# Optimization experiments

Measured on AMD Instinct MI355X. Metric: run time of the kernel, lower is better.

The kernel has to match this reference:

```python
import jax, jax.numpy as jnp
import numpy as np

B, D, H, W = 32, 64, 32, 32   # batch, laten_dim, latent spatial dims
K = 2048                      # codebook_size


def setup_inputs() -> dict:
    key = jax.random.key(0)
    k1, k2 = jax.random.split(key)
    laten = jax.random.normal(k1, (B, D, H, W), dtype=jnp.float32)
    codebook = jax.random.normal(k2, (K, D), dtype=jnp.float32)
    return {"laten": laten, "codebook": codebook}


def reference(laten, codebook):
    # Faithful jax translation of VQVAE.quant_laten.
    b, c, h, w = laten.shape
    # (b, c, h, w) -> (b*h*w, c)
    x = jnp.transpose(laten, (0, 2, 3, 1)).reshape(-1, c)  # (N, D)
    # avoids materializing the (N, K, D) broadcast intermediate.
    x_sq = jnp.sum(x * x, axis=-1, keepdims=True)          # (N, 1)
    e_sq = jnp.sum(codebook * codebook, axis=-1)           # (K,)
    l2_distance = (x_sq - 2.0 * (x @ codebook.T) + e_sq) / c  # (N, K)
    closest_idx_2d = jnp.argmin(l2_distance, axis=-1).reshape(b, h, w)
    # gather + permute(0, 3, 1, 2)
    quant_laten = jnp.transpose(codebook[closest_idx_2d], (0, 3, 1, 2))
    return closest_idx_2d, quant_laten
```

## Files before the change

kernel.cpp:

```cpp
#include <hip/hip_runtime.h>

#define N_PIX 32768
#define DIM   64
#define KCODE 2048

typedef __attribute__((ext_vector_type(8))) short bf16x8;
typedef __attribute__((ext_vector_type(4))) float f32x4;

__device__ inline unsigned short f2bf(float v) {
    unsigned int u = __float_as_uint(v);
    return (unsigned short)((u + 0x7FFFu + ((u >> 16) & 1u)) >> 16);
}
__device__ inline float bf2f(unsigned short b) {
    return __uint_as_float(((unsigned int)b) << 16);
}

__global__ __launch_bounds__(256)
void convert_b_kernel(const float* __restrict__ cb, unsigned short* __restrict__ Bg,
                      float* __restrict__ esq) {
    const int t   = blockIdx.x * 256 + threadIdx.x;
    const int n   = t >> 4;
    const int sub = t & 15;
    const int ntile = n >> 4, ni = n & 15;

    const float4 v = *(const float4*)(cb + (size_t)n * DIM + sub * 4);

    unsigned int h01, h23, m01, m23, l01, l23;
    {
        unsigned short h, m, l;
        float r1;
        h = f2bf(v.x); r1 = v.x - bf2f(h); m = f2bf(r1); l = f2bf(r1 - bf2f(m));
        h01 = h;       m01 = m;       l01 = l;
        h = f2bf(v.y); r1 = v.y - bf2f(h); m = f2bf(r1); l = f2bf(r1 - bf2f(m));
        h01 |= (unsigned int)h << 16; m01 |= (unsigned int)m << 16; l01 |= (unsigned int)l << 16;
        h = f2bf(v.z); r1 = v.z - bf2f(h); m = f2bf(r1); l = f2bf(r1 - bf2f(m));
        h23 = h;       m23 = m;       l23 = l;
        h = f2bf(v.w); r1 = v.w - bf2f(h); m = f2bf(r1); l = f2bf(r1 - bf2f(m));
        h23 |= (unsigned int)h << 16; m23 |= (unsigned int)m << 16; l23 |= (unsigned int)l << 16;
    }

    float s = (v.x * v.x + v.y * v.y) + (v.z * v.z + v.w * v.w);
#pragma unroll
    for (int mk = 1; mk < 16; mk <<= 1) s += __shfl_xor(s, mk, 16);
    if (sub == 0) esq[n] = s;

    char* outb = (char*)Bg;
    const size_t u = ((((size_t)ntile) * 8 + (sub >> 1)) << 8) + ni * 16 + (sub & 1) * 8;
    uint2 hw2 = {h01, h23}, mw2 = {m01, m23}, lw2 = {l01, l23};
    *(uint2*)(outb + u)          = hw2;
    *(uint2*)(outb + 262144 + u) = mw2;
    *(uint2*)(outb + 524288 + u) = lw2;
}

#define DO_PASS(APL, BPL)                                                    \
    _Pragma("unroll") for (int ks = 0; ks < 2; ++ks)                         \
    _Pragma("unroll") for (int mt = 0; mt < 4; ++mt)                         \
        acc[mt] = __builtin_amdgcn_mfma_f32_16x16x32_bf16(                   \
            af[APL][mt][ks], bfr[BPL][ks], acc[mt], 0, 0, 0);

#define RELOAD(PL, JN)                                                       \
    if ((JN) < 32) {                                                         \
      const char* gb = bp0 + (size_t)(JN) * 2048 + (size_t)(PL) * 262144;    \
      bfr[PL][0] = *(const bf16x8*)(gb);                                     \
      bfr[PL][1] = *(const bf16x8*)(gb + 1024);                              \
    }

#define ITER(J)                                                              \
  {                                                                          \
    f32x4 acc[4];                                                            \
    acc[0] = f32x4{0.f, 0.f, 0.f, 0.f};                                      \
    acc[1] = f32x4{0.f, 0.f, 0.f, 0.f};                                      \
    acc[2] = f32x4{0.f, 0.f, 0.f, 0.f};                                      \
    acc[3] = f32x4{0.f, 0.f, 0.f, 0.f};                                      \
    __builtin_amdgcn_s_setprio(1);                                           \
    DO_PASS(0, 2)                                                            \
    RELOAD(2, (J) + 1)                                                       \
    DO_PASS(2, 0)                                                            \
    DO_PASS(1, 1)                                                            \
    DO_PASS(0, 1)                                                            \
    RELOAD(1, (J) + 1)                                                       \
    DO_PASS(1, 0)                                                            \
    DO_PASS(0, 0)                                                            \
    RELOAD(0, (J) + 1)                                                       \
    __builtin_amdgcn_s_setprio(0);                                           \
    const int n = wn * 512 + (J) * 16 + col;                                 \
    const float e = esqS[n];                                                 \
    _Pragma("unroll") for (int mt = 0; mt < 4; ++mt)                         \
    _Pragma("unroll") for (int r = 0; r < 4; ++r) {                          \
      float d = fmaf(-2.f, acc[mt][r], e);                                   \
      if (d < best[mt][r]) { best[mt][r] = d; bidx[mt][r] = n; }             \
    }                                                                        \
  }

__global__ __launch_bounds__(256, 2)
void dist_fused_kernel(const float* __restrict__ laten,
                       const unsigned short* __restrict__ Bg,
                       const float* __restrict__ esq,
                       const float* __restrict__ cb,
                       float* __restrict__ out0, float* __restrict__ out1) {
    __shared__ __align__(16) char ring[24576];
    __shared__ float esqS[2048];

    const int tid  = threadIdx.x;
    const int lane = tid & 63;
    const int wn   = tid >> 6;
    const int quad = lane >> 4, col = lane & 15;
    const int bx = blockIdx.x;
    const int bb = bx >> 4, hw0 = (bx & 15) * 64;

    const char* BgB = (const char*)Bg;
    const char* bp0 = BgB + (size_t)(wn * 32) * 2048 + lane * 16;

    {
        const int p = tid & 63, dgp = tid >> 6;
        const int mt = p >> 4, mi = p & 15;
#pragma unroll
        for (int dd = 0; dd < 2; ++dd) {
            const int dg = dgp * 2 + dd;
            const float* srcA = laten + (size_t)bb * 65536 + (size_t)dg * 8192 + hw0 + p;
            alignas(16) unsigned short hv[8], mv[8], lv[8];
#pragma unroll
            for (int j = 0; j < 8; ++j) {
                float v = srcA[(size_t)j << 10];
                unsigned short h = f2bf(v);
                float r1 = v - bf2f(h);
                unsigned short m = f2bf(r1);
                unsigned short l = f2bf(r1 - bf2f(m));
                hv[j] = h; mv[j] = m; lv[j] = l;
            }
            int u = ((mt * 8 + dg) << 8) + mi * 16;
            *(uint4*)(ring + u)         = *(uint4*)hv;
            *(uint4*)(ring + 8192 + u)  = *(uint4*)mv;
            *(uint4*)(ring + 16384 + u) = *(uint4*)lv;
        }
    }
    *(float4*)(esqS + tid * 8)     = *(const float4*)(esq + tid * 8);
    *(float4*)(esqS + tid * 8 + 4) = *(const float4*)(esq + tid * 8 + 4);
    __syncthreads();

    bf16x8 af[3][4][2];
#pragma unroll
    for (int pl = 0; pl < 3; ++pl)
#pragma unroll
        for (int mt = 0; mt < 4; ++mt)
#pragma unroll
            for (int ks = 0; ks < 2; ++ks)
                af[pl][mt][ks] = *(const bf16x8*)(ring + pl * 8192
                    + ((mt * 8 + ks * 4 + quad) << 8) + col * 16);
    __syncthreads();

    bf16x8 bfr[3][2];
    RELOAD(2, 0)
    RELOAD(0, 0)
    RELOAD(1, 0)

    float best[4][4];
    int   bidx[4][4];
#pragma unroll
    for (int mt = 0; mt < 4; ++mt)
#pragma unroll
        for (int r = 0; r < 4; ++r) { best[mt][r] = 3.4e38f; bidx[mt][r] = 0; }

    for (int j = 0; j < 32; ++j) ITER(j)

    float* redD = (float*)ring;
    int*   redI = (int*)(ring + 1024);
    int*   idxF = (int*)(ring + 2048);
#pragma unroll
    for (int mt = 0; mt < 4; ++mt)
#pragma unroll
        for (int r = 0; r < 4; ++r) {
            float d = best[mt][r];
            int   i = bidx[mt][r];
#pragma unroll
            for (int m = 1; m < 16; m <<= 1) {
                float od = __shfl_xor(d, m, 16);
                int   oi = __shfl_xor(i, m, 16);
                if (od < d || (od == d && oi < i)) { d = od; i = oi; }
            }
            if (col == 0) {
                int row = mt * 16 + quad * 4 + r;
                redD[row * 4 + wn] = d;
                redI[row * 4 + wn] = i;
            }
        }
    __syncthreads();

    if (tid < 64) {
        float bd = redD[tid * 4]; int bi = redI[tid * 4];
#pragma unroll
        for (int w = 1; w < 4; ++w) {
            float d = redD[tid * 4 + w]; int i = redI[tid * 4 + w];
            if (d < bd || (d == bd && i < bi)) { bd = d; bi = i; }
        }
        out0[bx * 64 + tid] = (float)bi;
        idxF[tid] = bi;
    }
    __syncthreads();

    const int p = tid & 63, dgp = tid >> 6;
    const int idx = idxF[p];
    const float4* srcr = (const float4*)(cb + ((size_t)idx << 6) + dgp * 16);
    float* o = out1 + (size_t)bb * 65536 + (size_t)dgp * 16384 + hw0 + p;
    float4 v0 = srcr[0], v1 = srcr[1], v2 = srcr[2], v3 = srcr[3];
    o[(size_t)0  << 10] = v0.x; o[(size_t)1  << 10] = v0.y;
    o[(size_t)2  << 10] = v0.z; o[(size_t)3  << 10] = v0.w;
    o[(size_t)4  << 10] = v1.x; o[(size_t)5  << 10] = v1.y;
    o[(size_t)6  << 10] = v1.z; o[(size_t)7  << 10] = v1.w;
    o[(size_t)8  << 10] = v2.x; o[(size_t)9  << 10] = v2.y;
    o[(size_t)10 << 10] = v2.z; o[(size_t)11 << 10] = v2.w;
    o[(size_t)12 << 10] = v3.x; o[(size_t)13 << 10] = v3.y;
    o[(size_t)14 << 10] = v3.z; o[(size_t)15 << 10] = v3.w;
}

extern "C" void kernel_launch(void* const* d_in, const int* in_sizes, int n_in,
                              void* d_out, int out_size, void* d_ws, size_t ws_size,
                              hipStream_t stream) {
    const float* laten = (const float*)d_in[0];
    const float* cb    = (const float*)d_in[1];

    float* out0 = (float*)d_out;
    float* out1 = (float*)d_out + N_PIX;

    float* esq = (float*)d_ws;
    unsigned short* Bg = (unsigned short*)(esq + 2048);

    convert_b_kernel<<<128, 256, 0, stream>>>(cb, Bg, esq);

    dist_fused_kernel<<<512, 256, 0, stream>>>(laten, Bg, esq, cb, out0, out1);
}
```

Baseline: 103.5 us.

## Double-buffer MFMA accumulators to overlap argmin with next tile's matmul

Measured after the change: 229.4 us. 2.22x slower.

```diff
diff --git a/kernel.cpp b/kernel.cpp
--- a/kernel.cpp
+++ b/kernel.cpp
@@ -52,11 +52,11 @@
     *(uint2*)(outb + 524288 + u) = lw2;
 }
 
-#define DO_PASS(APL, BPL)                                                    \
+#define DO_PASS(APL, BPL, ACC)                                               \
     _Pragma("unroll") for (int ks = 0; ks < 2; ++ks)                         \
     _Pragma("unroll") for (int mt = 0; mt < 4; ++mt)                         \
-        acc[mt] = __builtin_amdgcn_mfma_f32_16x16x32_bf16(                   \
-            af[APL][mt][ks], bfr[BPL][ks], acc[mt], 0, 0, 0);
+        ACC[mt] = __builtin_amdgcn_mfma_f32_16x16x32_bf16(                   \
+            af[APL][mt][ks], bfr[BPL][ks], ACC[mt], 0, 0, 0);
 
 #define RELOAD(PL, JN)                                                       \
     if ((JN) < 32) {                                                         \
@@ -65,29 +65,32 @@
       bfr[PL][1] = *(const bf16x8*)(gb + 1024);                              \
     }
 
-#define ITER(J)                                                              \
+#define MB(J, ACC, DOREL)                                                    \
   {                                                                          \
-    f32x4 acc[4];                                                            \
-    acc[0] = f32x4{0.f, 0.f, 0.f, 0.f};                                      \
-    acc[1] = f32x4{0.f, 0.f, 0.f, 0.f};                                      \
-    acc[2] = f32x4{0.f, 0.f, 0.f, 0.f};                                      \
-    acc[3] = f32x4{0.f, 0.f, 0.f, 0.f};                                      \
+    ACC[0] = f32x4{0.f, 0.f, 0.f, 0.f};                                      \
+    ACC[1] = f32x4{0.f, 0.f, 0.f, 0.f};                                      \
+    ACC[2] = f32x4{0.f, 0.f, 0.f, 0.f};                                      \
+    ACC[3] = f32x4{0.f, 0.f, 0.f, 0.f};                                      \
     __builtin_amdgcn_s_setprio(1);                                           \
-    DO_PASS(0, 2)                                                            \
-    RELOAD(2, (J) + 1)                                                       \
-    DO_PASS(2, 0)                                                            \
-    DO_PASS(1, 1)                                                            \
-    DO_PASS(0, 1)                                                            \
-    RELOAD(1, (J) + 1)                                                       \
-    DO_PASS(1, 0)                                                            \
-    DO_PASS(0, 0)                                                            \
-    RELOAD(0, (J) + 1)                                                       \
+    DO_PASS(0, 2, ACC)                                                       \
+    if (DOREL) RELOAD(2, (J) + 1)                                            \
+    DO_PASS(2, 0, ACC)                                                       \
+    DO_PASS(1, 1, ACC)                                                       \
+    DO_PASS(0, 1, ACC)                                                       \
+    if (DOREL) RELOAD(1, (J) + 1)                                            \
+    DO_PASS(1, 0, ACC)                                                       \
+    DO_PASS(0, 0, ACC)                                                       \
+    if (DOREL) RELOAD(0, (J) + 1)                                            \
     __builtin_amdgcn_s_setprio(0);                                           \
+  }
+
+#define AM(ACC, J)                                                           \
+  {                                                                          \
     const int n = wn * 512 + (J) * 16 + col;                                 \
     const float e = esqS[n];                                                 \
     _Pragma("unroll") for (int mt = 0; mt < 4; ++mt)                         \
     _Pragma("unroll") for (int r = 0; r < 4; ++r) {                          \
-      float d = fmaf(-2.f, acc[mt][r], e);                                   \
+      float d = fmaf(-2.f, ACC[mt][r], e);                                   \
       if (d < best[mt][r]) { best[mt][r] = d; bidx[mt][r] = n; }             \
     }                                                                        \
   }
@@ -144,9 +147,11 @@
 #pragma unroll
         for (int mt = 0; mt < 4; ++mt)
 #pragma unroll
-            for (int ks = 0; ks < 2; ++ks)
+            for (int ks = 0; ks < 2; ++ks) {
                 af[pl][mt][ks] = *(const bf16x8*)(ring + pl * 8192
                     + ((mt * 8 + ks * 4 + quad) << 8) + col * 16);
+                asm volatile("" : "+v"(af[pl][mt][ks]));
+            }
     __syncthreads();
 
     bf16x8 bfr[3][2];
@@ -161,7 +166,18 @@
 #pragma unroll
         for (int r = 0; r < 4; ++r) { best[mt][r] = 3.4e38f; bidx[mt][r] = 0; }
 
-    for (int j = 0; j < 32; ++j) ITER(j)
+    f32x4 accA[4], accB[4];
+    MB(0, accA, 1)
+#pragma unroll
+    for (int t = 0; t < 30; t += 2) {
+        MB(t + 1, accB, 1)
+        AM(accA, t)
+        MB(t + 2, accA, 1)
+        AM(accB, t + 1)
+    }
+    MB(31, accB, 0)
+    AM(accA, 30)
+    AM(accB, 31)
 
     float* redD = (float*)ring;
     int*   redI = (int*)(ring + 1024);
```
